# Optimization experiments

Measured on AMD Instinct MI355X. Metric: run time of the kernel, lower is better.

The kernel has to match this reference:

```python
import jax, jax.numpy as jnp
import numpy as np

NEG_SLOPE = 0.2  # PyG GATConv leaky_relu slope


def _gat_conv(x, src, dst, W, a_s, a_d, b, H, D, concat):
    """PyG-style GATConv (eval mode, self-loops already in src/dst).
    x: [N, F_in], W: [F_in, H*D], a_s/a_d: [H, D], b: [H*D] or [D]."""
    N = x.shape[0]
    h = (x @ W).reshape(N, H, D)                      # [N, H, D]
    al_src = (h * a_s).sum(-1)                        # [N, H]
    al_dst = (h * a_d).sum(-1)                        # [N, H]
    e = jax.nn.leaky_relu(al_src[src] + al_dst[dst], NEG_SLOPE)   # [E, H]
    m = jax.ops.segment_max(e, dst, num_segments=N)               # [N, H]
    m = jnp.where(jnp.isfinite(m), m, 0.0)
    ex = jnp.exp(e - m[dst])
    denom = jax.ops.segment_sum(ex, dst, num_segments=N)
    alpha = ex / (denom[dst] + 1e-16)                 # edge softmax per dst node
    out = jax.ops.segment_sum(alpha[:, :, None] * h[src], dst, num_segments=N)  # [N, H, D]
    out = out.reshape(N, H * D) if concat else out.mean(axis=1)
    return out + b


def setup_inputs() -> dict:
    key = jax.random.key(0)
    ks = jax.random.split(key, 14)
    N, E, F_in, H, D, OUT = 50000, 800000, 256, 8, 32, 64
    g = lambda k, shape, fan: (jax.random.normal(k, shape, jnp.float32) / np.float32(np.sqrt(fan)))
    return {
        "x": jax.random.normal(ks[0], (N, F_in), jnp.float32),
        "edge_index": jax.random.randint(ks[1], (2, E), 0, N),
        # conv0: GATConv(256 -> 32, heads=8, concat)
        "W0": g(ks[2], (F_in, H * D), F_in),
        "a_src0": g(ks[3], (H, D), D),
        "a_dst0": g(ks[4], (H, D), D),
        "b0": jnp.zeros((H * D,), jnp.float32),
        # residual0: Linear(256 -> 256)
        "Wr0": g(ks[5], (F_in, H * D), F_in),
        "br0": jnp.zeros((H * D,), jnp.float32),
        # conv1: GATConv(256 -> 64, heads=1, concat=False)
        "W1": g(ks[6], (H * D, OUT), H * D),
        "a_src1": g(ks[7], (1, OUT), OUT),
        "a_dst1": g(ks[8], (1, OUT), OUT),
        "b1": jnp.zeros((OUT,), jnp.float32),
        # residual1: Linear(256 -> 64)
        "Wr1": g(ks[9], (H * D, OUT), H * D),
        "br1": jnp.zeros((OUT,), jnp.float32),
    }


def reference(x, edge_index, W0, a_src0, a_dst0, b0, Wr0, br0, W1, a_src1, a_dst1, b1, Wr1, br1):
    N = x.shape[0]
    loops = jnp.arange(N, dtype=edge_index.dtype)
    src = jnp.concatenate([edge_index[0], loops])   # add self loops
    dst = jnp.concatenate([edge_index[1], loops])
    # layer 0: GATConv + residual + ELU (dropout is identity in eval)
    h = _gat_conv(x, src, dst, W0, a_src0, a_dst0, b0, 8, 32, True)
    h = jax.nn.elu(h + (x @ Wr0 + br0))
    # final layer: heads=1, concat=False, + residual
    out = _gat_conv(h, src, dst, W1, a_src1, a_dst1, b1, 1, 64, False)
    out = out + (h @ Wr1 + br1)
    return jax.nn.log_softmax(out, axis=1)
```

## Files before the change

### kernel.cpp

```cpp
#include <hip/hip_runtime.h>
#include <math.h>

#define NEG_SLOPE 0.2f
#define BSH 7
#define NBLK_PART 256

typedef __attribute__((ext_vector_type(8))) short bf16x8;
typedef __attribute__((ext_vector_type(4))) float f32x4;
typedef __attribute__((ext_vector_type(2))) float f32x2;
typedef __attribute__((ext_vector_type(8))) unsigned short ushort8;
typedef __attribute__((ext_vector_type(4))) unsigned short ushort4v;

__device__ __forceinline__ float b2f(unsigned short u){
  return __uint_as_float(((unsigned)u) << 16);
}
__device__ __forceinline__ unsigned short f2b(float f){
  unsigned u = __float_as_uint(f);
  return (unsigned short)((u + 0x7FFFu + ((u >> 16) & 1u)) >> 16);
}

#if __has_builtin(__builtin_amdgcn_cvt_pk_f32_fp8) && __has_builtin(__builtin_amdgcn_cvt_pk_fp8_f32)
#define HW_FP8 1
#else
#define HW_FP8 0
#endif

#if !HW_FP8
__device__ __forceinline__ unsigned enc8_one(float f){
  unsigned bits = __float_as_uint(f);
  unsigned s = bits >> 31;
  unsigned e = (bits >> 23) & 255;
  unsigned mant = bits & 0x7FFFFF;
  if(e < 121){
    float af = fabsf(f);
    int m = (int)(af * 512.f + 0.5f);
    if(m > 7) m = 7;
    return (s << 7) | (unsigned)m;
  }
  unsigned lsb = (mant >> 20) & 1;
  mant += 0x7FFFF + lsb;
  if(mant >> 23){ e += 1; mant = 0; }
  unsigned m3 = mant >> 20;
  unsigned e8 = e - 120;
  if(e8 > 15 || (e8 == 15 && m3 == 7)) return (s << 7) | 0x7E;
  return (s << 7) | (e8 << 3) | m3;
}
#endif

template<bool HI>
__device__ __forceinline__ unsigned enc8_pair(float a, float b, unsigned old){
#if HW_FP8
  return __builtin_amdgcn_cvt_pk_fp8_f32(a, b, old, HI);
#else
  unsigned p = enc8_one(a) | (enc8_one(b) << 8);
  return HI ? ((old & 0x0000FFFFu) | (p << 16)) : ((old & 0xFFFF0000u) | p);
#endif
}

__device__ __forceinline__ void dec8x4v(unsigned q, f32x2& lo, f32x2& hi){
#if HW_FP8
  lo = __builtin_amdgcn_cvt_pk_f32_fp8(q, false);
  hi = __builtin_amdgcn_cvt_pk_f32_fp8(q, true);
#else
  auto dec1 = [](unsigned b)->float{
    unsigned s = (b >> 7) & 1, e = (b >> 3) & 15, m = b & 7;
    float v = (e == 0) ? (float)m * 0.001953125f
                       : __uint_as_float(((e + 120) << 23) | (m << 20));
    return s ? -v : v;
  };
  lo[0] = dec1(q & 255); lo[1] = dec1((q >> 8) & 255);
  hi[0] = dec1((q >> 16) & 255); hi[1] = dec1(q >> 24);
#endif
}

extern "C" __global__ void k_part1(const int* __restrict__ dsts, int E, int N,
                                   int NBUCK, int* __restrict__ bcnt,
                                   int* __restrict__ blockbase){
  __shared__ int hist[512];
  int blk = blockIdx.x, tid = threadIdx.x;
  for(int b = tid; b < NBUCK; b += 256) hist[b] = 0;
  __syncthreads();
  int ET = E + N;
  int chunk = (ET + NBLK_PART - 1)/NBLK_PART;
  int s0 = blk*chunk, s1 = s0+chunk < ET ? s0+chunk : ET;
  for(int e = s0+tid; e < s1; e += 256){
    int d = (e < E) ? dsts[e] : e - E;
    atomicAdd(&hist[d >> BSH], 1);
  }
  __syncthreads();
  for(int b = tid; b < NBUCK; b += 256)
    blockbase[(size_t)blk*NBUCK + b] = atomicAdd(&bcnt[b], hist[b]);
}

extern "C" __global__ void k_bscan(const int* __restrict__ bcnt, int* __restrict__ boffs,
                                   int* __restrict__ offs_last, int NBUCK, int ET){
  __shared__ int sc[512], orig[512];
  int t = threadIdx.x;
  int v = (t < NBUCK) ? bcnt[t] : 0;
  sc[t] = v; orig[t] = v;
  __syncthreads();
  for(int st=1; st<512; st<<=1){
    int u = (t >= st) ? sc[t-st] : 0;
    __syncthreads();
    sc[t] += u;
    __syncthreads();
  }
  if(t < NBUCK) boffs[t] = sc[t] - orig[t];
  if(t == 0){ boffs[NBUCK] = ET; *offs_last = ET; }
}

extern "C" __global__ void k_part2(const int* __restrict__ srcs, const int* __restrict__ dsts,
                                   int E, int N, int NBUCK,
                                   const int* __restrict__ boffs, const int* __restrict__ blockbase,
                                   unsigned* __restrict__ pairs){
  __shared__ int cur[512];
  int blk = blockIdx.x, tid = threadIdx.x;
  for(int b = tid; b < NBUCK; b += 256)
    cur[b] = boffs[b] + blockbase[(size_t)blk*NBUCK + b];
  __syncthreads();
  int ET = E + N;
  int chunk = (ET + NBLK_PART - 1)/NBLK_PART;
  int s0 = blk*chunk, s1 = s0+chunk < ET ? s0+chunk : ET;
  for(int e = s0+tid; e < s1; e += 256){
    int s, d;
    if(e < E){ s = srcs[e]; d = dsts[e]; } else { s = d = e - E; }
    int pos = atomicAdd(&cur[d >> BSH], 1);
    pairs[pos] = ((unsigned)s << 7) | ((unsigned)d & 127u);
  }
}

extern "C" __global__ void k_bcsr(const unsigned* __restrict__ pairs, const int* __restrict__ boffs,
                                  int N, int* __restrict__ offs, int* __restrict__ csr){
  __shared__ int hist[128], sc[128], lcur[128];
  int b = blockIdx.x, tid = threadIdx.x;
  int node0 = b << BSH;
  int base = boffs[b], endp = boffs[b+1];
  if(tid < 128) hist[tid] = 0;
  __syncthreads();
  for(int i = base + tid; i < endp; i += 256)
    atomicAdd(&hist[pairs[i] & 127u], 1);
  __syncthreads();
  if(tid < 128) sc[tid] = hist[tid];
  __syncthreads();
  for(int st=1; st<128; st<<=1){
    int u = (tid < 128 && tid >= st) ? sc[tid-st] : 0;
    __syncthreads();
    if(tid < 128) sc[tid] += u;
    __syncthreads();
  }
  if(tid < 128){
    int ex = sc[tid] - hist[tid];
    lcur[tid] = ex;
    int n = node0 + tid;
    if(n < N) offs[n] = base + ex;
  }
  __syncthreads();
  for(int i = base + tid; i < endp; i += 256){
    unsigned pr = pairs[i];
    int pos = atomicAdd(&lcur[pr & 127u], 1);
    csr[base + pos] = (int)(pr >> 7);
  }
}

extern "C" __global__ void k_wt2(const float* __restrict__ W0, const float* __restrict__ Wr0,
                                 const float* __restrict__ W1, const float* __restrict__ Wr1,
                                 unsigned short* __restrict__ WT0, unsigned short* __restrict__ WT1){
  int idx = blockIdx.x*256 + threadIdx.x;
  const int tot0 = 512*256;
  if(idx < tot0){
    int n = idx >> 8, k = idx & 255;
    const float* W = (n < 256) ? W0 : Wr0;
    int c = (n < 256) ? n : n - 256;
    WT0[idx] = f2b(W[(size_t)k*256 + c]);
  } else {
    idx -= tot0;
    if(idx >= 128*256) return;
    int n = idx >> 8, k = idx & 255;
    const float* W = (n < 64) ? W1 : Wr1;
    int c = (n < 64) ? n : n - 64;
    WT1[idx] = f2b(W[(size_t)k*64 + c]);
  }
}

__launch_bounds__(256)
extern "C" __global__ void k_mgemm0(const float* __restrict__ Afp,
                                    const unsigned short* __restrict__ WT,
                                    int M, int MB,
                                    unsigned char* __restrict__ qout,
                                    unsigned short* __restrict__ rout,
                                    const float* __restrict__ asv, const float* __restrict__ adv,
                                    float* __restrict__ alsout, float* __restrict__ aldout){
  int id = blockIdx.x;
  int col_blk = (id >> 3) & 3;
  int row_blk = (id >> 5)*8 + (id & 7);
  if(row_blk >= MB) return;

  __shared__ unsigned short SH[24576];
  unsigned short* As = SH;
  int t = threadIdx.x;
  int lane = t & 63, wid = t >> 6;
  int wr = wid >> 1, wc = wid & 1;
  int row0 = row_blk*128, col0 = col_blk*128;
  f32x4 acc[4][4] = {};

  float4 v0s[4], v1s[4];
  const float* abase[4];
  #pragma unroll
  for(int i=0; i<4; i++){
    int t2 = i*256 + t;
    int r = t2 >> 3, dslot = (t2 & 7) ^ (r & 7);
    int gr = row0 + r; if(gr >= M) gr = M - 1;
    abase[i] = Afp + (size_t)gr*256 + dslot*8;
    v0s[i] = *(const float4*)(abase[i]);
    v1s[i] = *(const float4*)(abase[i] + 4);
  }
  #pragma unroll
  for(int i=0; i<4; i++){
    int t2 = i*256 + t;
    int r = t2 >> 3, dslot = (t2 & 7) ^ (r & 7);
    const unsigned short* gb = WT + (size_t)(col0 + r)*256 + dslot*8;
    __builtin_amdgcn_global_load_lds((const __attribute__((address_space(1))) unsigned*)gb,
        (__attribute__((address_space(3))) unsigned*)(SH + 8192 + i*2048 + wid*512), 16, 0, 0);
  }

  #pragma unroll
  for(int ks=0; ks<4; ks++){
    const int k0 = ks*64;
    unsigned short* Bc = SH + 8192 + (ks & 1)*8192;
    unsigned short* Bn = SH + 8192 + ((ks & 1) ^ 1)*8192;
    #pragma unroll
    for(int i=0; i<4; i++){
      ushort8 o;
      o[0]=f2b(v0s[i].x); o[1]=f2b(v0s[i].y); o[2]=f2b(v0s[i].z); o[3]=f2b(v0s[i].w);
      o[4]=f2b(v1s[i].x); o[5]=f2b(v1s[i].y); o[6]=f2b(v1s[i].z); o[7]=f2b(v1s[i].w);
      *(ushort8*)(As + i*2048 + wid*512 + lane*8) = o;
    }
    __syncthreads();
    if(ks < 3){
      #pragma unroll
      for(int i=0; i<4; i++){
        int t2 = i*256 + t;
        int r = t2 >> 3, dslot = (t2 & 7) ^ (r & 7);
        const unsigned short* gb = WT + (size_t)(col0 + r)*256 + (k0 + 64) + dslot*8;
        __builtin_amdgcn_global_load_lds((const __attribute__((address_space(1))) unsigned*)gb,
            (__attribute__((address_space(3))) unsigned*)(Bn + i*2048 + wid*512), 16, 0, 0);
      }
      #pragma unroll
      for(int i=0; i<4; i++){
        v0s[i] = *(const float4*)(abase[i] + k0 + 64);
        v1s[i] = *(const float4*)(abase[i] + k0 + 68);
      }
    }
    #pragma unroll
    for(int kc=0; kc<2; kc++){
      bf16x8 a[4], b[4];
      int kb = kc*4 + (lane >> 4);
      #pragma unroll
      for(int f=0; f<4; f++){
        int ar = wr*64 + f*16 + (lane & 15);
        a[f] = *(const bf16x8*)&As[ar*64 + ((kb ^ (ar & 7))*8)];
        int br = wc*64 + f*16 + (lane & 15);
        b[f] = *(const bf16x8*)&Bc[br*64 + ((kb ^ (br & 7))*8)];
      }
      #pragma unroll
      for(int fm=0; fm<4; fm++)
        #pragma unroll
        for(int fn=0; fn<4; fn++)
          acc[fm][fn] = __builtin_amdgcn_mfma_f32_16x16x32_bf16(a[fm], b[fn], acc[fm][fn], 0, 0, 0);
    }
    __syncthreads();
  }

  unsigned short* CT = SH;
  int cg = t & 15;
  bool attn = col_blk < 2;
  int colbase = col0 + cg*8;
  float4 as_lo, as_hi, ad_lo, ad_hi;
  if(attn){
    as_lo = *(const float4*)(asv + colbase);
    as_hi = *(const float4*)(asv + colbase + 4);
    ad_lo = *(const float4*)(adv + colbase);
    ad_hi = *(const float4*)(adv + colbase + 4);
  }
  #pragma unroll
  for(int half=0; half<2; half++){
    __syncthreads();
    if(wr == half){
      #pragma unroll
      for(int fm=0; fm<4; fm++){
        int rbase = fm*16 + ((lane>>4)<<2);
        #pragma unroll
        for(int r=0; r<4; r++)
          #pragma unroll
          for(int fn=0; fn<4; fn++)
            CT[(rbase+r)*136 + wc*64 + (lane&15) + fn*16] = f2b(acc[fm][fn][r]);
      }
    }
    __syncthreads();
    #pragma unroll
    for(int it=0; it<4; it++){
      int rl = it*16 + (t>>4);
      int row = row0 + half*64 + rl;
      ushort8 vr = *(ushort8*)&CT[rl*136 + cg*8];
      if(attn){
        float f0=b2f(vr[0]),f1=b2f(vr[1]),f2=b2f(vr[2]),f3=b2f(vr[3]);
        float f4=b2f(vr[4]),f5=b2f(vr[5]),f6=b2f(vr[6]),f7=b2f(vr[7]);
        float sd = f0*as_lo.x+f1*as_lo.y+f2*as_lo.z+f3*as_lo.w
                 + f4*as_hi.x+f5*as_hi.y+f6*as_hi.z+f7*as_hi.w;
        float dd = f0*ad_lo.x+f1*ad_lo.y+f2*ad_lo.z+f3*ad_lo.w
                 + f4*ad_hi.x+f5*ad_hi.y+f6*ad_hi.z+f7*ad_hi.w;
        sd += __shfl_xor(sd,1); sd += __shfl_xor(sd,2);
        dd += __shfl_xor(dd,1); dd += __shfl_xor(dd,2);
        uint2 q;
        q.x = enc8_pair<false>(f0,f1,0u); q.x = enc8_pair<true>(f2,f3,q.x);
        q.y = enc8_pair<false>(f4,f5,0u); q.y = enc8_pair<true>(f6,f7,q.y);
        if(row < M){
          *(uint2*)(qout + (size_t)row*256 + colbase) = q;
          if((t&3)==0){
            int head = colbase >> 5;
            alsout[row*8 + head] = sd;
            aldout[row*8 + head] = dd;
          }
        }
      } else {
        if(row < M)
          *(ushort8*)(rout + (size_t)row*256 + (colbase - 256)) = vr;
      }
    }
  }
}

__launch_bounds__(256)
extern "C" __global__ void k_mgemm1(const unsigned short* __restrict__ Ab,
                                    const unsigned short* __restrict__ WT,
                                    unsigned short* __restrict__ C, int M, int MB,
                                    unsigned char* __restrict__ qout,
                                    const float* __restrict__ asv, const float* __restrict__ adv,
                                    float* __restrict__ alsout, float* __restrict__ aldout){
  int row_blk = blockIdx.x;
  if(row_blk >= MB) return;

  __shared__ unsigned short SH[128*128];
  unsigned short* As = SH;
  unsigned short* Bs = SH + 128*64;
  int t = threadIdx.x;
  int lane = t & 63, wid = t >> 6;
  int wr = wid >> 1, wc = wid & 1;
  int row0 = row_blk*128;
  f32x4 acc[4][4] = {};

  for(int k0 = 0; k0 < 256; k0 += 64){
    #pragma unroll
    for(int i=0; i<4; i++){
      int t2 = i*256 + t;
      int r = t2 >> 3;
      int dslot = (t2 & 7) ^ (r & 7);
      int gr = row0 + r; if(gr >= M) gr = M - 1;
      const unsigned short* ga = Ab + (size_t)gr*256 + k0 + dslot*8;
      __builtin_amdgcn_global_load_lds((const __attribute__((address_space(1))) unsigned*)ga,
          (__attribute__((address_space(3))) unsigned*)(As + i*2048 + wid*512), 16, 0, 0);
      const unsigned short* gb = WT + (size_t)r*256 + k0 + dslot*8;
      __builtin_amdgcn_global_load_lds((const __attribute__((address_space(1))) unsigned*)gb,
          (__attribute__((address_space(3))) unsigned*)(Bs + i*2048 + wid*512), 16, 0, 0);
    }
    __syncthreads();
    #pragma unroll
    for(int kc=0; kc<2; kc++){
      bf16x8 a[4], b[4];
      int kb = kc*4 + (lane >> 4);
      #pragma unroll
      for(int f=0; f<4; f++){
        int ar = wr*64 + f*16 + (lane & 15);
        a[f] = *(const bf16x8*)&As[ar*64 + ((kb ^ (ar & 7))*8)];
        int br = wc*64 + f*16 + (lane & 15);
        b[f] = *(const bf16x8*)&Bs[br*64 + ((kb ^ (br & 7))*8)];
      }
      #pragma unroll
      for(int fm=0; fm<4; fm++)
        #pragma unroll
        for(int fn=0; fn<4; fn++)
          acc[fm][fn] = __builtin_amdgcn_mfma_f32_16x16x32_bf16(a[fm], b[fn], acc[fm][fn], 0, 0, 0);
    }
    __syncthreads();
  }

  unsigned short* CT = SH;
  int cg = t & 15;
  #pragma unroll
  for(int half=0; half<2; half++){
    __syncthreads();
    if(wr == half){
      #pragma unroll
      for(int fm=0; fm<4; fm++){
        int rbase = fm*16 + ((lane>>4)<<2);
        #pragma unroll
        for(int r=0; r<4; r++)
          #pragma unroll
          for(int fn=0; fn<4; fn++)
            CT[(rbase+r)*136 + wc*64 + (lane&15) + fn*16] = f2b(acc[fm][fn][r]);
      }
    }
    __syncthreads();
    #pragma unroll
    for(int it=0; it<4; it++){
      int rl = it*16 + (t>>4);
      int row = row0 + half*64 + rl;
      ushort8 vr = *(ushort8*)&CT[rl*136 + cg*8];
      if(row < M){
        *(ushort8*)(C + (size_t)row*128 + cg*8) = vr;
        if(cg < 8){
          float f0=b2f(vr[0]),f1=b2f(vr[1]),f2=b2f(vr[2]),f3=b2f(vr[3]);
          float f4=b2f(vr[4]),f5=b2f(vr[5]),f6=b2f(vr[6]),f7=b2f(vr[7]);
          uint2 q;
          q.x = enc8_pair<false>(f0,f1,0u); q.x = enc8_pair<true>(f2,f3,q.x);
          q.y = enc8_pair<false>(f4,f5,0u); q.y = enc8_pair<true>(f6,f7,q.y);
          *(uint2*)(qout + (size_t)row*64 + cg*8) = q;
          float sd = f0*asv[cg*8+0]+f1*asv[cg*8+1]+f2*asv[cg*8+2]+f3*asv[cg*8+3]
                   + f4*asv[cg*8+4]+f5*asv[cg*8+5]+f6*asv[cg*8+6]+f7*asv[cg*8+7];
          float dd = f0*adv[cg*8+0]+f1*adv[cg*8+1]+f2*adv[cg*8+2]+f3*adv[cg*8+3]
                   + f4*adv[cg*8+4]+f5*adv[cg*8+5]+f6*adv[cg*8+6]+f7*adv[cg*8+7];
          sd += __shfl_xor(sd,1); sd += __shfl_xor(sd,2); sd += __shfl_xor(sd,4);
          dd += __shfl_xor(dd,1); dd += __shfl_xor(dd,2); dd += __shfl_xor(dd,4);
          if((t&15)==0){
            alsout[row] = sd;
            aldout[row] = dd;
          }
        }
      }
    }
  }
}

__launch_bounds__(256)
extern "C" __global__ void k_gather0(const unsigned short* __restrict__ r0b,
                                     const unsigned char* __restrict__ h0q,
                                     const float* __restrict__ als0, const float* __restrict__ ald0,
                                     const int* __restrict__ offs, const int* __restrict__ csr,
                                     const float* __restrict__ b0, const float* __restrict__ br0,
                                     unsigned short* __restrict__ h1b, int N){
  int n = blockIdx.x*4 + (threadIdx.x >> 6);
  if(n >= N) return;
  int lane = threadIdx.x & 63;
  int hh = lane & 7;
  int es = lane >> 3;
  int h  = es;
  int c  = lane*4;
  float ald_h = ald0[n*8 + hh];
  int beg = offs[n], end = offs[n+1];

  f32x2 A01 = {0.f, 0.f}, A23 = {0.f, 0.f};
  float den = 0.f;

  for(int chunk = beg; chunk < end; chunk += 8){
    int m = end - chunk; if(m > 8) m = 8;
    bool e_ok = es < m;
    int s = e_ok ? csr[chunk + es] : 0;
    float p = 0.f;
    if(e_ok){
      float v = als0[s*8 + hh] + ald_h;
      v = v > 0.f ? v : NEG_SLOPE*v;
      p = expf(v);
    }
    den += p;
    int sj[8]; float pj[8];
    #pragma unroll
    for(int j=0; j<8; j++){
      sj[j] = __shfl(s, j*8);
      pj[j] = __shfl(p, j*8 + h);
    }
    unsigned q[8];
    #pragma unroll
    for(int j=0; j<8; j++)
      q[j] = *(const unsigned*)(h0q + (size_t)sj[j]*256 + c);
    #pragma unroll
    for(int j=0; j<8; j++){
      f32x2 lo, hi, pv;
      dec8x4v(q[j], lo, hi);
      pv[0] = pj[j]; pv[1] = pj[j];
      A01 += pv*lo; A23 += pv*hi;
    }
  }

  den += __shfl_xor(den, 8);
  den += __shfl_xor(den, 16);
  den += __shfl_xor(den, 32);
  float rden = 1.f/(den + 1e-16f);
  rden = __shfl(rden, h);

  float a0 = A01[0]*rden, a1 = A01[1]*rden, a2 = A23[0]*rden, a3 = A23[1]*rden;

  float4 bb = *(const float4*)(b0 + c);
  float4 rb = *(const float4*)(br0 + c);
  uint2 ru = *(const uint2*)(r0b + (size_t)n*256 + c);
  float o0 = a0 + bb.x + __uint_as_float(ru.x << 16)         + rb.x;
  float o1 = a1 + bb.y + __uint_as_float(ru.x & 0xFFFF0000u) + rb.y;
  float o2 = a2 + bb.z + __uint_as_float(ru.y << 16)         + rb.z;
  float o3 = a3 + bb.w + __uint_as_float(ru.y & 0xFFFF0000u) + rb.w;
  ushort4v o;
  o[0] = f2b(o0 > 0.f ? o0 : expf(o0) - 1.f);
  o[1] = f2b(o1 > 0.f ? o1 : expf(o1) - 1.f);
  o[2] = f2b(o2 > 0.f ? o2 : expf(o2) - 1.f);
  o[3] = f2b(o3 > 0.f ? o3 : expf(o3) - 1.f);
  *(ushort4v*)(h1b + (size_t)n*256 + c) = o;
}

__launch_bounds__(256)
extern "C" __global__ void k_gather1(const unsigned short* __restrict__ buf1b,
                                     const unsigned char* __restrict__ g1q,
                                     const float* __restrict__ als1, const float* __restrict__ ald1,
                                     const int* __restrict__ offs, const int* __restrict__ csr,
                                     const float* __restrict__ b1, const float* __restrict__ br1,
                                     float* __restrict__ out, int N){
  int n = blockIdx.x*4 + (threadIdx.x >> 6);
  if(n >= N) return;
  int lane = threadIdx.x & 63;
  int ch4 = lane & 15;
  int es  = lane >> 4;
  int c   = ch4*4;
  int beg = offs[n], end = offs[n+1];
  float ald_n = ald1[n];

  f32x2 A01 = {0.f, 0.f}, A23 = {0.f, 0.f};
  float den = 0.f;

  for(int chunk = beg; chunk < end; chunk += 64){
    int m = end - chunk; if(m > 64) m = 64;
    int s = (lane < m) ? csr[chunk + lane] : 0;
    float p = 0.f;
    if(lane < m){
      float v = als1[s] + ald_n;
      v = v > 0.f ? v : NEG_SLOPE*v;
      p = expf(v);
    }
    den += p;
    for(int base = 0; base < m; base += 16){
      int sv[4]; float pv[4];
      #pragma unroll
      for(int i=0; i<4; i++){
        int j = base + 4*i + es;
        int jj = j & 63;
        sv[i] = __shfl(s, jj);
        pv[i] = __shfl(p, jj);
      }
      unsigned qv[4];
      #pragma unroll
      for(int i=0; i<4; i++)
        qv[i] = *(const unsigned*)(g1q + (size_t)sv[i]*64 + c);
      #pragma unroll
      for(int i=0; i<4; i++){
        f32x2 lo, hi, pp;
        dec8x4v(qv[i], lo, hi);
        pp[0] = pv[i]; pp[1] = pv[i];
        A01 += pp*lo; A23 += pp*hi;
      }
    }
  }

  A01[0] += __shfl_xor(A01[0], 16); A01[1] += __shfl_xor(A01[1], 16);
  A23[0] += __shfl_xor(A23[0], 16); A23[1] += __shfl_xor(A23[1], 16);
  A01[0] += __shfl_xor(A01[0], 32); A01[1] += __shfl_xor(A01[1], 32);
  A23[0] += __shfl_xor(A23[0], 32); A23[1] += __shfl_xor(A23[1], 32);
  #pragma unroll
  for(int o=32; o>0; o>>=1) den += __shfl_xor(den, o);
  float rden = 1.f/(den + 1e-16f);

  float4 bb = *(const float4*)(b1 + c);
  float4 rb = *(const float4*)(br1 + c);
  uint2 ru = *(const uint2*)(buf1b + (size_t)n*128 + 64 + c);
  float v0 = A01[0]*rden + bb.x + __uint_as_float(ru.x << 16)         + rb.x;
  float v1 = A01[1]*rden + bb.y + __uint_as_float(ru.x & 0xFFFF0000u) + rb.y;
  float v2 = A23[0]*rden + bb.z + __uint_as_float(ru.y << 16)         + rb.z;
  float v3 = A23[1]*rden + bb.w + __uint_as_float(ru.y & 0xFFFF0000u) + rb.w;

  float mx = fmaxf(fmaxf(v0, v1), fmaxf(v2, v3));
  #pragma unroll
  for(int o=1; o<16; o<<=1) mx = fmaxf(mx, __shfl_xor(mx, o));
  float sm = expf(v0-mx) + expf(v1-mx) + expf(v2-mx) + expf(v3-mx);
  #pragma unroll
  for(int o=1; o<16; o<<=1) sm += __shfl_xor(sm, o);
  float l = mx + logf(sm);
  if(es == 0){
    float4 ov; ov.x = v0-l; ov.y = v1-l; ov.z = v2-l; ov.w = v3-l;
    *(float4*)(out + (size_t)n*64 + c) = ov;
  }
}

extern "C" void kernel_launch(void* const* d_in, const int* in_sizes, int n_in,
                              void* d_out, int out_size, void* d_ws, size_t ws_size,
                              hipStream_t stream){
  const float* x   = (const float*)d_in[0];
  const int*   ei  = (const int*)  d_in[1];
  const float* W0  = (const float*)d_in[2];
  const float* as0 = (const float*)d_in[3];
  const float* ad0 = (const float*)d_in[4];
  const float* b0  = (const float*)d_in[5];
  const float* Wr0 = (const float*)d_in[6];
  const float* br0 = (const float*)d_in[7];
  const float* W1  = (const float*)d_in[8];
  const float* as1 = (const float*)d_in[9];
  const float* ad1 = (const float*)d_in[10];
  const float* b1  = (const float*)d_in[11];
  const float* Wr1 = (const float*)d_in[12];
  const float* br1 = (const float*)d_in[13];
  int N = in_sizes[0] / 256;
  int E = in_sizes[1] / 2;
  const int* srcs = ei;
  const int* dsts = ei + E;
  float* out = (float*)d_out;

  int ET = E + N;
  int NBUCK = (N + 127) >> BSH;

  unsigned short* r0b   = (unsigned short*)d_ws;
  unsigned char*  h0q   = (unsigned char*)(r0b + (size_t)N*256);
  unsigned short* h1b   = (unsigned short*)(h0q + (size_t)N*256);
  unsigned short* buf1b = h1b + (size_t)N*256;
  unsigned short* WT0   = buf1b + (size_t)N*128;
  unsigned short* WT1   = WT0   + 512*256;
  float*    als0 = (float*)(WT1 + 128*256);
  float*    ald0 = als0 + (size_t)N*8;
  float*    als1 = ald0 + (size_t)N*8;
  float*    ald1 = als1 + N;
  int*      offs = (int*)(ald1 + N);
  int*      bcnt = offs + N + 1;
  int*      boffs = bcnt + NBUCK;
  int*      blockbase = boffs + NBUCK + 1;
  int*      csr  = blockbase + (size_t)NBLK_PART*NBUCK;
  unsigned* pairs = (unsigned*)(csr + ET);
  unsigned char* g1q = (unsigned char*)(pairs + ET);

  hipMemsetAsync(bcnt, 0, (size_t)NBUCK*sizeof(int), stream);
  hipLaunchKernelGGL(k_part1, dim3(NBLK_PART), dim3(256), 0, stream, dsts, E, N, NBUCK, bcnt, blockbase);
  hipLaunchKernelGGL(k_bscan, dim3(1), dim3(512), 0, stream, bcnt, boffs, offs + N, NBUCK, ET);
  hipLaunchKernelGGL(k_part2, dim3(NBLK_PART), dim3(256), 0, stream, srcs, dsts, E, N, NBUCK, boffs, blockbase, pairs);
  hipLaunchKernelGGL(k_bcsr, dim3(NBUCK), dim3(256), 0, stream, pairs, boffs, N, offs, csr);

  hipLaunchKernelGGL(k_wt2, dim3((512*256+128*256+255)/256), dim3(256), 0, stream, W0, Wr0, W1, Wr1, WT0, WT1);

  int MB = (N + 127) / 128;
  int g0 = ((MB + 7) / 8) * 32;
  hipLaunchKernelGGL(k_mgemm0, dim3(g0), dim3(256), 0, stream,
                     x, WT0, N, MB, h0q, r0b, as0, ad0, als0, ald0);
  hipLaunchKernelGGL(k_gather0, dim3((N+3)/4), dim3(256), 0, stream, r0b, h0q, als0, ald0, offs, csr, b0, br0, h1b, N);

  hipLaunchKernelGGL(k_mgemm1, dim3(MB), dim3(256), 0, stream,
                     h1b, WT1, buf1b, N, MB, g1q, as1, ad1, als1, ald1);
  hipLaunchKernelGGL(k_gather1, dim3((N+3)/4), dim3(256), 0, stream, buf1b, g1q, als1, ald1, offs, csr, b1, br1, out, N);
}
```

Before: 183.3 us.

## Split fp8 feature table into per-XCD head slices and single-buffer GEMM B tile

The layer-0 fp8 feature table is stored as four column slices of 64 bytes per node, each a 3.2MB table. The gather kernel maps blocks so each XCD handles one slice, which keeps that slice resident in its L2 and lets each wave process 16 edges per step across 16 lanes. The GEMM drops double-buffered B loads in favour of a single buffer loaded each k-step. That shrinks LDS use but serialises B loads with compute, and the gather adds cross-lane reductions and issues four times as many blocks.

```diff
diff --git a/kernel.cpp b/kernel.cpp
--- a/kernel.cpp
+++ b/kernel.cpp
@@ -195,8 +195,9 @@
   int row_blk = (id >> 5)*8 + (id & 7);
   if(row_blk >= MB) return;
 
-  __shared__ unsigned short SH[24576];
+  __shared__ unsigned short SH[128*128];
   unsigned short* As = SH;
+  unsigned short* Bs = SH + 128*64;
   int t = threadIdx.x;
   int lane = t & 63, wid = t >> 6;
   int wr = wid >> 1, wc = wid & 1;
@@ -214,20 +215,8 @@
     v0s[i] = *(const float4*)(abase[i]);
     v1s[i] = *(const float4*)(abase[i] + 4);
   }
-  #pragma unroll
-  for(int i=0; i<4; i++){
-    int t2 = i*256 + t;
-    int r = t2 >> 3, dslot = (t2 & 7) ^ (r & 7);
-    const unsigned short* gb = WT + (size_t)(col0 + r)*256 + dslot*8;
-    __builtin_amdgcn_global_load_lds((const __attribute__((address_space(1))) unsigned*)gb,
-        (__attribute__((address_space(3))) unsigned*)(SH + 8192 + i*2048 + wid*512), 16, 0, 0);
-  }
-
-  #pragma unroll
-  for(int ks=0; ks<4; ks++){
-    const int k0 = ks*64;
-    unsigned short* Bc = SH + 8192 + (ks & 1)*8192;
-    unsigned short* Bn = SH + 8192 + ((ks & 1) ^ 1)*8192;
+
+  for(int k0 = 0; k0 < 256; k0 += 64){
     #pragma unroll
     for(int i=0; i<4; i++){
       ushort8 o;
@@ -235,16 +224,16 @@
       o[4]=f2b(v1s[i].x); o[5]=f2b(v1s[i].y); o[6]=f2b(v1s[i].z); o[7]=f2b(v1s[i].w);
       *(ushort8*)(As + i*2048 + wid*512 + lane*8) = o;
     }
-    __syncthreads();
-    if(ks < 3){
-      #pragma unroll
-      for(int i=0; i<4; i++){
-        int t2 = i*256 + t;
-        int r = t2 >> 3, dslot = (t2 & 7) ^ (r & 7);
-        const unsigned short* gb = WT + (size_t)(col0 + r)*256 + (k0 + 64) + dslot*8;
-        __builtin_amdgcn_global_load_lds((const __attribute__((address_space(1))) unsigned*)gb,
-            (__attribute__((address_space(3))) unsigned*)(Bn + i*2048 + wid*512), 16, 0, 0);
-      }
+    #pragma unroll
+    for(int i=0; i<4; i++){
+      int t2 = i*256 + t;
+      int r = t2 >> 3, dslot = (t2 & 7) ^ (r & 7);
+      const unsigned short* gb = WT + (size_t)(col0 + r)*256 + k0 + dslot*8;
+      __builtin_amdgcn_global_load_lds((const __attribute__((address_space(1))) unsigned*)gb,
+          (__attribute__((address_space(3))) unsigned*)(Bs + i*2048 + wid*512), 16, 0, 0);
+    }
+    __syncthreads();
+    if(k0 < 192){
       #pragma unroll
       for(int i=0; i<4; i++){
         v0s[i] = *(const float4*)(abase[i] + k0 + 64);
@@ -260,7 +249,7 @@
         int ar = wr*64 + f*16 + (lane & 15);
         a[f] = *(const bf16x8*)&As[ar*64 + ((kb ^ (ar & 7))*8)];
         int br = wc*64 + f*16 + (lane & 15);
-        b[f] = *(const bf16x8*)&Bc[br*64 + ((kb ^ (br & 7))*8)];
+        b[f] = *(const bf16x8*)&Bs[br*64 + ((kb ^ (br & 7))*8)];
       }
       #pragma unroll
       for(int fm=0; fm<4; fm++)
@@ -275,6 +264,8 @@
   int cg = t & 15;
   bool attn = col_blk < 2;
   int colbase = col0 + cg*8;
+  int qt = colbase >> 6;
+  int qcol = colbase & 63;
   float4 as_lo, as_hi, ad_lo, ad_hi;
   if(attn){
     as_lo = *(const float4*)(asv + colbase);
@@ -315,7 +306,7 @@
         q.x = enc8_pair<false>(f0,f1,0u); q.x = enc8_pair<true>(f2,f3,q.x);
         q.y = enc8_pair<false>(f4,f5,0u); q.y = enc8_pair<true>(f6,f7,q.y);
         if(row < M){
-          *(uint2*)(qout + (size_t)row*256 + colbase) = q;
+          *(uint2*)(qout + (size_t)qt*M*64 + (size_t)row*64 + qcol) = q;
           if((t&3)==0){
             int head = colbase >> 5;
             alsout[row*8 + head] = sd;
@@ -438,70 +429,87 @@
                                      const int* __restrict__ offs, const int* __restrict__ csr,
                                      const float* __restrict__ b0, const float* __restrict__ br0,
                                      unsigned short* __restrict__ h1b, int N){
-  int n = blockIdx.x*4 + (threadIdx.x >> 6);
+  int i = blockIdx.x;
+  int xcd = i & 7;
+  int qt = xcd >> 1, parity = xcd & 1;
+  int j = i >> 3;
+  int n = (j*2 + parity)*4 + (threadIdx.x >> 6);
   if(n >= N) return;
   int lane = threadIdx.x & 63;
-  int hh = lane & 7;
-  int es = lane >> 3;
-  int h  = es;
-  int c  = lane*4;
-  float ald_h = ald0[n*8 + hh];
+  int ch4 = lane & 15;
+  int es  = lane >> 4;
+  int hb  = lane & 1;
+  int hbc = ch4 >> 3;
+  const unsigned char* tab = h0q + (size_t)qt*N*64;
+  float ald_h = ald0[n*8 + qt*2 + hb];
   int beg = offs[n], end = offs[n+1];
 
   f32x2 A01 = {0.f, 0.f}, A23 = {0.f, 0.f};
   float den = 0.f;
 
-  for(int chunk = beg; chunk < end; chunk += 8){
-    int m = end - chunk; if(m > 8) m = 8;
-    bool e_ok = es < m;
-    int s = e_ok ? csr[chunk + es] : 0;
+  for(int chunk = beg; chunk < end; chunk += 32){
+    int m = end - chunk; if(m > 32) m = 32;
+    int el = lane >> 1;
+    int s = (el < m) ? csr[chunk + el] : 0;
     float p = 0.f;
-    if(e_ok){
-      float v = als0[s*8 + hh] + ald_h;
+    if(el < m){
+      float v = als0[s*8 + qt*2 + hb] + ald_h;
       v = v > 0.f ? v : NEG_SLOPE*v;
       p = expf(v);
     }
     den += p;
-    int sj[8]; float pj[8];
-    #pragma unroll
-    for(int j=0; j<8; j++){
-      sj[j] = __shfl(s, j*8);
-      pj[j] = __shfl(p, j*8 + h);
-    }
-    unsigned q[8];
-    #pragma unroll
-    for(int j=0; j<8; j++)
-      q[j] = *(const unsigned*)(h0q + (size_t)sj[j]*256 + c);
-    #pragma unroll
-    for(int j=0; j<8; j++){
-      f32x2 lo, hi, pv;
-      dec8x4v(q[j], lo, hi);
-      pv[0] = pj[j]; pv[1] = pj[j];
-      A01 += pv*lo; A23 += pv*hi;
-    }
-  }
-
+    for(int base = 0; base < m; base += 16){
+      int sv[4]; float pv[4];
+      #pragma unroll
+      for(int ii=0; ii<4; ii++){
+        int jj = base + 4*ii + es;
+        int sl = (jj & 31)*2;
+        sv[ii] = __shfl(s, sl);
+        float px = __shfl(p, sl + hbc);
+        pv[ii] = (jj < m) ? px : 0.f;
+      }
+      unsigned qv[4];
+      #pragma unroll
+      for(int ii=0; ii<4; ii++)
+        qv[ii] = *(const unsigned*)(tab + (size_t)sv[ii]*64 + ch4*4);
+      #pragma unroll
+      for(int ii=0; ii<4; ii++){
+        f32x2 lo, hi, pp;
+        dec8x4v(qv[ii], lo, hi);
+        pp[0] = pv[ii]; pp[1] = pv[ii];
+        A01 += pp*lo; A23 += pp*hi;
+      }
+    }
+  }
+
+  A01[0] += __shfl_xor(A01[0], 16); A01[1] += __shfl_xor(A01[1], 16);
+  A23[0] += __shfl_xor(A23[0], 16); A23[1] += __shfl_xor(A23[1], 16);
+  A01[0] += __shfl_xor(A01[0], 32); A01[1] += __shfl_xor(A01[1], 32);
+  A23[0] += __shfl_xor(A23[0], 32); A23[1] += __shfl_xor(A23[1], 32);
+  den += __shfl_xor(den, 2);
+  den += __shfl_xor(den, 4);
   den += __shfl_xor(den, 8);
   den += __shfl_xor(den, 16);
   den += __shfl_xor(den, 32);
-  float rden = 1.f/(den + 1e-16f);
-  rden = __shfl(rden, h);
-
-  float a0 = A01[0]*rden, a1 = A01[1]*rden, a2 = A23[0]*rden, a3 = A23[1]*rden;
-
+  float rdv = 1.f/(den + 1e-16f);
+  float rden = __shfl(rdv, hbc);
+
+  int c = qt*64 + ch4*4;
   float4 bb = *(const float4*)(b0 + c);
   float4 rb = *(const float4*)(br0 + c);
   uint2 ru = *(const uint2*)(r0b + (size_t)n*256 + c);
-  float o0 = a0 + bb.x + __uint_as_float(ru.x << 16)         + rb.x;
-  float o1 = a1 + bb.y + __uint_as_float(ru.x & 0xFFFF0000u) + rb.y;
-  float o2 = a2 + bb.z + __uint_as_float(ru.y << 16)         + rb.z;
-  float o3 = a3 + bb.w + __uint_as_float(ru.y & 0xFFFF0000u) + rb.w;
-  ushort4v o;
-  o[0] = f2b(o0 > 0.f ? o0 : expf(o0) - 1.f);
-  o[1] = f2b(o1 > 0.f ? o1 : expf(o1) - 1.f);
-  o[2] = f2b(o2 > 0.f ? o2 : expf(o2) - 1.f);
-  o[3] = f2b(o3 > 0.f ? o3 : expf(o3) - 1.f);
-  *(ushort4v*)(h1b + (size_t)n*256 + c) = o;
+  float o0 = A01[0]*rden + bb.x + __uint_as_float(ru.x << 16)         + rb.x;
+  float o1 = A01[1]*rden + bb.y + __uint_as_float(ru.x & 0xFFFF0000u) + rb.y;
+  float o2 = A23[0]*rden + bb.z + __uint_as_float(ru.y << 16)         + rb.z;
+  float o3 = A23[1]*rden + bb.w + __uint_as_float(ru.y & 0xFFFF0000u) + rb.w;
+  if(es == 0){
+    ushort4v o;
+    o[0] = f2b(o0 > 0.f ? o0 : expf(o0) - 1.f);
+    o[1] = f2b(o1 > 0.f ? o1 : expf(o1) - 1.f);
+    o[2] = f2b(o2 > 0.f ? o2 : expf(o2) - 1.f);
+    o[3] = f2b(o3 > 0.f ? o3 : expf(o3) - 1.f);
+    *(ushort4v*)(h1b + (size_t)n*256 + c) = o;
+  }
 }
 
 __launch_bounds__(256)
@@ -641,7 +649,8 @@
   int g0 = ((MB + 7) / 8) * 32;
   hipLaunchKernelGGL(k_mgemm0, dim3(g0), dim3(256), 0, stream,
                      x, WT0, N, MB, h0q, r0b, as0, ad0, als0, ald0);
-  hipLaunchKernelGGL(k_gather0, dim3((N+3)/4), dim3(256), 0, stream, r0b, h0q, als0, ald0, offs, csr, b0, br0, h1b, N);
+  int ggath = 8 * ((N + 7) / 8);
+  hipLaunchKernelGGL(k_gather0, dim3(ggath), dim3(256), 0, stream, r0b, h0q, als0, ald0, offs, csr, b0, br0, h1b, N);
 
   hipLaunchKernelGGL(k_mgemm1, dim3(MB), dim3(256), 0, stream,
                      h1b, WT1, buf1b, N, MB, g1q, as1, ad1, als1, ald1);
```

Result: slower. 231.7 us (+26.4%).
